# Optimization experiments

Measured on AMD Instinct MI355X. Metric: run time of the kernel, lower is better.

Reference implementation:

```python
import jax, jax.numpy as jnp
import numpy as np

G = 32          # grid size passed to FlashKAN
K_DEG = 3       # cubic B-splines
LO, HI = -3.0, 3.0

def make_knots():
    h = (HI - LO) / G
    # extended uniform knot vector: G + 2k + 1 knots -> G + k = 35 cubic basis fns
    return jnp.asarray(np.linspace(LO - K_DEG * h, HI + K_DEG * h, G + 2 * K_DEG + 1), jnp.float32)

def bspline_basis(x, knots):
    # Cox-de Boor, vectorized over all leading dims; loop only over degree (3 iters)
    xe = jnp.clip(x, LO, HI - 1e-4)[..., None]
    b = ((xe >= knots[:-1]) & (xe < knots[1:])).astype(x.dtype)  # degree-0 indicators
    for d in range(1, K_DEG + 1):
        left = (xe - knots[:-(d + 1)]) / (knots[d:-1] - knots[:-(d + 1)]) * b[..., :-1]
        right = (knots[d + 1:] - xe) / (knots[d + 1:] - knots[1:-d]) * b[..., 1:]
        b = left + right
    return b  # [..., E, G+K_DEG]

def kan(x, w_base, w_sp, knots):
    # FlashKAN layer: SiLU base branch + B-spline branch
    base = jax.nn.silu(x) @ w_base                          # [..., E] @ [E, O]
    spline = jnp.einsum('bleg,ego->blo', bspline_basis(x, knots), w_sp)
    return base + spline

def reference(query, key, value, wq_base, wq_sp, wk_base, wk_sp, wv_base, wv_sp):
    B, L, E = query.shape
    S = key.shape[-2]
    H = 8
    Dh = E // H
    knots = make_knots()
    Q = kan(query, wq_base, wq_sp, knots).reshape(B, L, H, Dh).transpose(0, 2, 1, 3)
    K = kan(key, wk_base, wk_sp, knots).reshape(B, S, H, Dh).transpose(0, 2, 1, 3)
    V = kan(value, wv_base, wv_sp, knots).reshape(B, S, H, Dh).transpose(0, 2, 1, 3)
    # no softmax, dropout p=0 -> (Q @ K^T) @ V == Q @ (K^T @ V), use O(L*d^2) form
    KtV = jnp.einsum('bhsd,bhse->bhde', K, V)               # [B,H,Dh,Dh]
    out = jnp.einsum('bhld,bhde->bhle', Q, KtV)             # [B,H,L,Dh]
    return out.transpose(0, 2, 1, 3).reshape(B, L, E)

def setup_inputs():
    key = jax.random.key(0)
    ks = jax.random.split(key, 9)
    B, L, E, NB = 2, 1024, 512, G + K_DEG
    sp_scale = 0.1 / np.sqrt(E)
    base_scale = 1.0 / np.sqrt(E)
    return {
        'query': jax.random.normal(ks[0], (B, L, E), jnp.float32),
        'key': jax.random.normal(ks[1], (B, L, E), jnp.float32),
        'value': jax.random.normal(ks[2], (B, L, E), jnp.float32),
        'wq_base': jax.random.normal(ks[3], (E, E), jnp.float32) * base_scale,
        'wq_sp': jax.random.normal(ks[4], (E, NB, E), jnp.float32) * sp_scale,
        'wk_base': jax.random.normal(ks[5], (E, E), jnp.float32) * base_scale,
        'wk_sp': jax.random.normal(ks[6], (E, NB, E), jnp.float32) * sp_scale,
        'wv_base': jax.random.normal(ks[7], (E, E), jnp.float32) * base_scale,
        'wv_sp': jax.random.normal(ks[8], (E, NB, E), jnp.float32) * sp_scale,
    }
```

## Files before the change

### kernel.cpp

```cpp
#include <hip/hip_runtime.h>
#include <hip/hip_bf16.h>
#include <stdint.h>

#define E_DIM 512
#define GNB   35
#define KSP   17920
#define KAUG  18432
#define MTOK  2048
#define BKW   128
#define NWIN  144
#define WINB  140
#define BM    128
#define BN    128
#define RB    256

typedef __attribute__((ext_vector_type(8))) short  short8;
typedef __attribute__((ext_vector_type(4))) short  short4v;
typedef __attribute__((ext_vector_type(4))) float  floatx4;

__device__ __forceinline__ short f2bf(float f) {
  __hip_bfloat16 h = __float2bfloat16(f);
  return *reinterpret_cast<short*>(&h);
}
__device__ __forceinline__ float silu_f(float x) { return x / (1.0f + __expf(-x)); }

__device__ __forceinline__ void gload_lds16(const void* g, void* l) {
  typedef const __attribute__((address_space(1))) void* gp_t;
  typedef __attribute__((address_space(3))) void* lp_t;
  __builtin_amdgcn_global_load_lds((gp_t)g, (lp_t)l, 16, 0, 0);
}

__device__ __forceinline__ int swz(int row, int byte_off) {
  return row * RB + (byte_off ^ ((row & 7) << 4));
}

__global__ __launch_bounds__(256) void wconv_kernel(
    const float* __restrict__ wq_sp, const float* __restrict__ wq_base,
    const float* __restrict__ wk_sp, const float* __restrict__ wk_base,
    const float* __restrict__ wv_sp, const float* __restrict__ wv_base,
    __hip_bfloat16* __restrict__ waugT)
{
  __shared__ float tile[64][65];
  const int tz = blockIdx.z;
  const float* wsp = tz == 0 ? wq_sp : (tz == 1 ? wk_sp : wv_sp);
  const float* wb  = tz == 0 ? wq_base : (tz == 1 ? wk_base : wv_base);
  const int k0 = blockIdx.x * 64;
  const int o0 = blockIdx.y * 64;
  const int t  = threadIdx.x;
#pragma unroll
  for (int it = 0; it < 16; ++it) {
    int idx = it * 256 + t;
    int r = idx >> 6, c = idx & 63;
    int k = k0 + r;
    float val = (k < KSP) ? wsp[(size_t)k * E_DIM + (o0 + c)]
                          : wb[(size_t)(k - KSP) * E_DIM + (o0 + c)];
    tile[r][c] = val;
  }
  __syncthreads();
  __hip_bfloat16* dst = waugT + (size_t)tz * E_DIM * KAUG;
#pragma unroll
  for (int it = 0; it < 16; ++it) {
    int idx = it * 256 + t;
    int r = idx >> 6, c = idx & 63;
    dst[(size_t)(o0 + r) * KAUG + (k0 + c)] = __float2bfloat16(tile[c][r]);
  }
}

template<int MODE>
__global__ __launch_bounds__(256) void kan_gemm(
    const float* __restrict__ q, const float* __restrict__ k_in,
    const float* __restrict__ v, const __hip_bfloat16* __restrict__ waugT,
    const float* __restrict__ wq_sp, const float* __restrict__ wq_base,
    const float* __restrict__ wk_sp, const float* __restrict__ wk_base,
    const float* __restrict__ wv_sp, const float* __restrict__ wv_base,
    float* __restrict__ C)
{
  __shared__ int4 sAq[BM * 16];
  __shared__ int4 sBq[BN * 16];
  char* pA = (char*)sAq;
  char* pB = (char*)sBq;

  const int z  = blockIdx.z;
  const int tz = z >> 2;
  const int ks = z & 3;
  const float* X = tz == 0 ? q : (tz == 1 ? k_in : v);
  const float* Wsp = tz == 0 ? wq_sp : (tz == 1 ? wk_sp : wv_sp);
  const float* Wb  = tz == 0 ? wq_base : (tz == 1 ? wk_base : wv_base);
  const char* WTb = (const char*)(waugT + (size_t)tz * E_DIM * KAUG);
  float* Cout = C + (size_t)tz * MTOK * E_DIM;

  const int m0 = blockIdx.x * BM;
  const int n0 = blockIdx.y * BN;
  const int t = threadIdx.x;
  const int lane = t & 63, wid = t >> 6;
  const int wm = wid >> 1, wn = wid & 1;
  const int fr = lane & 15, kg = lane >> 4;

  floatx4 acc[4][4];
  const floatx4 zf = {0.f, 0.f, 0.f, 0.f};
#pragma unroll
  for (int i = 0; i < 4; ++i)
#pragma unroll
    for (int j = 0; j < 4; ++j) acc[i][j] = zf;

  const int w_lo = ks * (NWIN / 4), w_hi = w_lo + (NWIN / 4);
  for (int win = w_lo; win < w_hi; ++win) {
    const int k0 = win * BKW;
    const bool spline = (win < WINB);
    __syncthreads();

    if (MODE == 0) {
      const int rB = t >> 4;
      const int cb = (t & 15) * 16;
#pragma unroll
      for (int p = 0; p < 8; ++p) {
        int row = p * 16 + rB;
        size_t goff = ((size_t)(n0 + row) * KAUG + k0) * 2
                    + (size_t)(cb ^ ((row & 7) << 4));
        gload_lds16(WTb + goff, pB + row * RB + cb);
      }
    } else {
      const float* Wrow = spline ? Wsp : Wb;
      const int koff0 = spline ? k0 : k0 - KSP;
      const int g  = t & 31;
      const int rg = t >> 5;
#pragma unroll
      for (int p = 0; p < 4; ++p) {
        const int r0 = (p * 8 + rg) * 4;
        float rv[4][4];
#pragma unroll
        for (int j = 0; j < 4; ++j) {
          const float* src = &Wrow[(size_t)(koff0 + r0 + j) * E_DIM + n0 + g];
#pragma unroll
          for (int j2 = 0; j2 < 4; ++j2) rv[j][j2] = src[32 * j2];
        }
#pragma unroll
        for (int j2 = 0; j2 < 4; ++j2) {
          const int nloc = g + 32 * j2;
          short4v sv;
          sv.x = f2bf(rv[0][j2]); sv.y = f2bf(rv[1][j2]);
          sv.z = f2bf(rv[2][j2]); sv.w = f2bf(rv[3][j2]);
          *(short4v*)&pB[swz(nloc, 2 * r0)] = sv;
        }
      }
    }

    if (spline) {
      const int4 z4 = make_int4(0, 0, 0, 0);
#pragma unroll
      for (int p = 0; p < 8; ++p) sAq[p * 256 + t] = z4;
      __syncthreads();
      const int elo = k0 / GNB;
      int ehi = (k0 + BKW - 1) / GNB; if (ehi > 511) ehi = 511;
      const int ne = ehi - elo + 1;
      const int npairs = BM * ne;
      for (int p = t; p < npairs; p += 256) {
        int m, ei;
        if (ne == 4) { m = p >> 2; ei = p & 3; }
        else         { m = (p * 52429) >> 18; ei = p - m * 5; }
        const int e = elo + ei;
        float x = X[(size_t)(m0 + m) * E_DIM + e];
        x = fminf(fmaxf(x, -3.0f), 3.0f - 1e-4f);
        float u = (x + 3.0f) * (16.0f / 3.0f);
        int ii = (int)u; ii = ii > 31 ? 31 : ii;
        float tt = u - (float)ii;
        float omt = 1.0f - tt;
        float t2 = tt * tt, t3 = t2 * tt;
        float b0 = omt * omt * omt * (1.0f / 6.0f);
        float b1 = (3.0f * t3 - 6.0f * t2 + 4.0f) * (1.0f / 6.0f);
        float b2 = (-3.0f * t3 + 3.0f * t2 + 3.0f * tt + 1.0f) * (1.0f / 6.0f);
        float b3 = t3 * (1.0f / 6.0f);
        const int c = e * GNB + ii - k0;
        if (c >= 0     && c < BKW)     *(short*)&pA[swz(m, 2 * c)]       = f2bf(b0);
        if (c + 1 >= 0 && c + 1 < BKW) *(short*)&pA[swz(m, 2 * (c + 1))] = f2bf(b1);
        if (c + 2 >= 0 && c + 2 < BKW) *(short*)&pA[swz(m, 2 * (c + 2))] = f2bf(b2);
        if (c + 3 >= 0 && c + 3 < BKW) *(short*)&pA[swz(m, 2 * (c + 3))] = f2bf(b3);
      }
    } else {
      const int e0 = k0 - KSP;
#pragma unroll
      for (int p = 0; p < 16; ++p) {
        int idx = p * 256 + t;
        int m = idx >> 5, c4 = idx & 31;
        floatx4 xv = *(const floatx4*)&X[(size_t)(m0 + m) * E_DIM + e0 + c4 * 4];
        short4v pk;
        pk.x = f2bf(silu_f(xv.x)); pk.y = f2bf(silu_f(xv.y));
        pk.z = f2bf(silu_f(xv.z)); pk.w = f2bf(silu_f(xv.w));
        *(short4v*)&pA[swz(m, 8 * c4)] = pk;
      }
    }
    __syncthreads();

#pragma unroll
    for (int kc = 0; kc < 4; ++kc) {
      const int kb = kc * 64 + kg * 16;
      short8 af[4], bfv[4];
#pragma unroll
      for (int fm = 0; fm < 4; ++fm) {
        const int row = wm * 64 + fm * 16 + fr;
        af[fm] = *(const short8*)&pA[swz(row, kb)];
      }
#pragma unroll
      for (int fn = 0; fn < 4; ++fn) {
        const int col = wn * 64 + fn * 16 + fr;
        bfv[fn] = *(const short8*)&pB[swz(col, kb)];
      }
#pragma unroll
      for (int fm = 0; fm < 4; ++fm)
#pragma unroll
        for (int fn = 0; fn < 4; ++fn)
          acc[fm][fn] = __builtin_amdgcn_mfma_f32_16x16x32_bf16(
              af[fm], bfv[fn], acc[fm][fn], 0, 0, 0);
    }
  }

  const int rowb = kg * 4;
#pragma unroll
  for (int fm = 0; fm < 4; ++fm)
#pragma unroll
    for (int fn = 0; fn < 4; ++fn)
#pragma unroll
      for (int r = 0; r < 4; ++r)
        atomicAdd(&Cout[(size_t)(m0 + wm * 64 + fm * 16 + rowb + r) * E_DIM
                        + (n0 + wn * 64 + fn * 16 + fr)],
                  acc[fm][fn][r]);
}

__global__ __launch_bounds__(256) void ktv_kernel(const float* __restrict__ C,
                                                  float* __restrict__ KtV)
{
  __shared__ float Ks[64][64];
  __shared__ float Vs[64][64];
  const int sc = blockIdx.x, bh = blockIdx.y;
  const int b = bh >> 3, h = bh & 7;
  const int t = threadIdx.x;
  const size_t base = ((size_t)(b * 1024 + sc * 64)) * E_DIM + h * 64;
  const float* Kp = C + (size_t)MTOK * E_DIM + base;
  const float* Vp = C + (size_t)2 * MTOK * E_DIM + base;
#pragma unroll
  for (int p = 0; p < 16; ++p) {
    int idx = p * 256 + t;
    int r = idx >> 6, c = idx & 63;
    Ks[r][c] = Kp[(size_t)r * E_DIM + c];
    Vs[r][c] = Vp[(size_t)r * E_DIM + c];
  }
  __syncthreads();
  const int d0 = (t & 15) * 4, e0 = (t >> 4) * 4;
  float acc[4][4] = {};
  for (int s = 0; s < 64; ++s) {
    float4 kv = *(const float4*)&Ks[s][d0];
    float4 vv = *(const float4*)&Vs[s][e0];
    float ka[4] = {kv.x, kv.y, kv.z, kv.w};
    float va[4] = {vv.x, vv.y, vv.z, vv.w};
#pragma unroll
    for (int i = 0; i < 4; ++i)
#pragma unroll
      for (int j = 0; j < 4; ++j) acc[i][j] = __fmaf_rn(ka[i], va[j], acc[i][j]);
  }
  float* dst = KtV + (size_t)bh * 4096;
#pragma unroll
  for (int i = 0; i < 4; ++i)
#pragma unroll
    for (int j = 0; j < 4; ++j)
      atomicAdd(&dst[(d0 + i) * 64 + (e0 + j)], acc[i][j]);
}

__global__ __launch_bounds__(256) void qktv_kernel(const float* __restrict__ C,
                                                   const float* __restrict__ KtV,
                                                   float* __restrict__ out)
{
  __shared__ float Qs[128][64];
  __shared__ float Ms[64][64];
  const int lt = blockIdx.x, bh = blockIdx.y;
  const int b = bh >> 3, h = bh & 7;
  const int t = threadIdx.x;
  const float* Qp = C + ((size_t)(b * 1024 + lt * 128)) * E_DIM + h * 64;
#pragma unroll
  for (int p = 0; p < 32; ++p) {
    int idx = p * 256 + t;
    Qs[idx >> 6][idx & 63] = Qp[(size_t)(idx >> 6) * E_DIM + (idx & 63)];
  }
#pragma unroll
  for (int p = 0; p < 16; ++p) {
    int idx = p * 256 + t;
    Ms[idx >> 6][idx & 63] = KtV[(size_t)bh * 4096 + idx];
  }
  __syncthreads();
  const int e0 = (t & 15) * 4;
  const int l0 = (t >> 4) * 8;
  float acc[8][4] = {};
  for (int d = 0; d < 64; ++d) {
    float4 mv = *(const float4*)&Ms[d][e0];
    float ma[4] = {mv.x, mv.y, mv.z, mv.w};
#pragma unroll
    for (int i = 0; i < 8; ++i) {
      float qv = Qs[l0 + i][d];
#pragma unroll
      for (int j = 0; j < 4; ++j) acc[i][j] = __fmaf_rn(qv, ma[j], acc[i][j]);
    }
  }
  float* op = out + ((size_t)(b * 1024 + lt * 128)) * E_DIM + h * 64;
#pragma unroll
  for (int i = 0; i < 8; ++i)
#pragma unroll
    for (int j = 0; j < 4; ++j)
      op[(size_t)(l0 + i) * E_DIM + (e0 + j)] = acc[i][j];
}

extern "C" void kernel_launch(void* const* d_in, const int* in_sizes, int n_in,
                              void* d_out, int out_size, void* d_ws, size_t ws_size,
                              hipStream_t stream) {
  const float* q   = (const float*)d_in[0];
  const float* k   = (const float*)d_in[1];
  const float* v   = (const float*)d_in[2];
  const float* wqb = (const float*)d_in[3];
  const float* wqs = (const float*)d_in[4];
  const float* wkb = (const float*)d_in[5];
  const float* wks = (const float*)d_in[6];
  const float* wvb = (const float*)d_in[7];
  const float* wvs = (const float*)d_in[8];

  char* ws = (char*)d_ws;
  const size_t WAUG_BYTES = (size_t)3 * E_DIM * KAUG * sizeof(__hip_bfloat16);
  const size_t C_BYTES    = (size_t)3 * MTOK * E_DIM * sizeof(float);
  const size_t KTV_BYTES  = (size_t)16 * 64 * 64 * sizeof(float);
  const bool full = ws_size >= WAUG_BYTES + C_BYTES + KTV_BYTES;
  float* C;
  float* KtV;
  __hip_bfloat16* waugT = (__hip_bfloat16*)ws;
  if (full) { C = (float*)(ws + WAUG_BYTES); KtV = (float*)(ws + WAUG_BYTES + C_BYTES); }
  else      { C = (float*)ws;                KtV = (float*)(ws + C_BYTES); }

  hipMemsetAsync(C, 0, C_BYTES, stream);
  hipMemsetAsync(KtV, 0, KTV_BYTES, stream);

  if (full) {
    wconv_kernel<<<dim3(KAUG / 64, E_DIM / 64, 3), 256, 0, stream>>>(
        wqs, wqb, wks, wkb, wvs, wvb, waugT);
    kan_gemm<0><<<dim3(MTOK / BM, E_DIM / BN, 12), 256, 0, stream>>>(
        q, k, v, waugT, wqs, wqb, wks, wkb, wvs, wvb, C);
  } else {
    kan_gemm<1><<<dim3(MTOK / BM, E_DIM / BN, 12), 256, 0, stream>>>(
        q, k, v, waugT, wqs, wqb, wks, wkb, wvs, wvb, C);
  }
  ktv_kernel<<<dim3(16, 16), 256, 0, stream>>>(C, KtV);
  qktv_kernel<<<dim3(8, 16), 256, 0, stream>>>(C, KtV, (float*)d_out);
}
```

Before: 431.7 us.

## Use k-slice LDS layout, XCD-aware block remap, vectorized weight conversion

Replaces the XOR-swizzled row-major LDS tiles with a k-slice-major layout, where each 8-element k chunk of all 128 rows is contiguous, so global_load_lds writes are linear per thread and MFMA fragment reads need no swizzle arithmetic. Flattens the GEMM grid to 1D and remaps block ids so consecutive blocks on the same XCD share weight and activation tiles for better L2 reuse. Vectorizes the weight conversion kernel with float4 loads and short4 bf16 stores. Replaces __syncthreads with explicit waitcnt plus s_barrier. The new layout may bring back LDS bank conflicts that the swizzle used to avoid.

```diff
diff --git a/kernel.cpp b/kernel.cpp
--- a/kernel.cpp
+++ b/kernel.cpp
@@ -12,7 +12,6 @@
 #define WINB  140
 #define BM    128
 #define BN    128
-#define RB    256
 
 typedef __attribute__((ext_vector_type(8))) short  short8;
 typedef __attribute__((ext_vector_type(4))) short  short4v;
@@ -30,9 +29,7 @@
   __builtin_amdgcn_global_load_lds((gp_t)g, (lp_t)l, 16, 0, 0);
 }
 
-__device__ __forceinline__ int swz(int row, int byte_off) {
-  return row * RB + (byte_off ^ ((row & 7) << 4));
-}
+__device__ __forceinline__ int kofs(int sl) { return ((sl >> 2) << 5) + ((sl & 3) << 3); }
 
 __global__ __launch_bounds__(256) void wconv_kernel(
     const float* __restrict__ wq_sp, const float* __restrict__ wq_base,
@@ -47,22 +44,26 @@
   const int k0 = blockIdx.x * 64;
   const int o0 = blockIdx.y * 64;
   const int t  = threadIdx.x;
-#pragma unroll
-  for (int it = 0; it < 16; ++it) {
+  const float* srcb = (k0 < KSP) ? wsp + (size_t)k0 * E_DIM
+                                 : wb + (size_t)(k0 - KSP) * E_DIM;
+#pragma unroll
+  for (int it = 0; it < 4; ++it) {
     int idx = it * 256 + t;
-    int r = idx >> 6, c = idx & 63;
-    int k = k0 + r;
-    float val = (k < KSP) ? wsp[(size_t)k * E_DIM + (o0 + c)]
-                          : wb[(size_t)(k - KSP) * E_DIM + (o0 + c)];
-    tile[r][c] = val;
+    int r = idx >> 4, c4 = (idx & 15) * 4;
+    floatx4 v = *(const floatx4*)&srcb[(size_t)r * E_DIM + o0 + c4];
+    tile[r][c4] = v.x; tile[r][c4 + 1] = v.y;
+    tile[r][c4 + 2] = v.z; tile[r][c4 + 3] = v.w;
   }
   __syncthreads();
   __hip_bfloat16* dst = waugT + (size_t)tz * E_DIM * KAUG;
 #pragma unroll
-  for (int it = 0; it < 16; ++it) {
+  for (int it = 0; it < 4; ++it) {
     int idx = it * 256 + t;
-    int r = idx >> 6, c = idx & 63;
-    dst[(size_t)(o0 + r) * KAUG + (k0 + c)] = __float2bfloat16(tile[c][r]);
+    int ro = idx >> 4, kc = (idx & 15) * 4;
+    short4v s;
+    s.x = f2bf(tile[kc][ro]);     s.y = f2bf(tile[kc + 1][ro]);
+    s.z = f2bf(tile[kc + 2][ro]); s.w = f2bf(tile[kc + 3][ro]);
+    *(short4v*)&dst[(size_t)(o0 + ro) * KAUG + k0 + kc] = s;
   }
 }
 
@@ -75,22 +76,25 @@
     const float* __restrict__ wv_sp, const float* __restrict__ wv_base,
     float* __restrict__ C)
 {
-  __shared__ int4 sAq[BM * 16];
-  __shared__ int4 sBq[BN * 16];
-  char* pA = (char*)sAq;
-  char* pB = (char*)sBq;
-
-  const int z  = blockIdx.z;
+  __shared__ char pA[32768];
+  __shared__ char pB[32768];
+
+  const int bid = blockIdx.x;
+  const int lid = (bid & 7) * 96 + (bid >> 3);
+  const int mx = lid & 15;
+  const int ny = (lid >> 4) & 3;
+  const int z  = lid >> 6;
   const int tz = z >> 2;
   const int ks = z & 3;
+
   const float* X = tz == 0 ? q : (tz == 1 ? k_in : v);
   const float* Wsp = tz == 0 ? wq_sp : (tz == 1 ? wk_sp : wv_sp);
   const float* Wb  = tz == 0 ? wq_base : (tz == 1 ? wk_base : wv_base);
   const char* WTb = (const char*)(waugT + (size_t)tz * E_DIM * KAUG);
   float* Cout = C + (size_t)tz * MTOK * E_DIM;
 
-  const int m0 = blockIdx.x * BM;
-  const int n0 = blockIdx.y * BN;
+  const int m0 = mx * BM;
+  const int n0 = ny * BN;
   const int t = threadIdx.x;
   const int lane = t & 63, wid = t >> 6;
   const int wm = wid >> 1, wn = wid & 1;
@@ -102,6 +106,9 @@
   for (int i = 0; i < 4; ++i)
 #pragma unroll
     for (int j = 0; j < 4; ++j) acc[i][j] = zf;
+
+  const int colt = t & 127;
+  const int slhi = t >> 7;
 
   const int w_lo = ks * (NWIN / 4), w_hi = w_lo + (NWIN / 4);
   for (int win = w_lo; win < w_hi; ++win) {
@@ -110,14 +117,11 @@
     __syncthreads();
 
     if (MODE == 0) {
-      const int rB = t >> 4;
-      const int cb = (t & 15) * 16;
 #pragma unroll
       for (int p = 0; p < 8; ++p) {
-        int row = p * 16 + rB;
-        size_t goff = ((size_t)(n0 + row) * KAUG + k0) * 2
-                    + (size_t)(cb ^ ((row & 7) << 4));
-        gload_lds16(WTb + goff, pB + row * RB + cb);
+        const int sl = 2 * p + slhi;
+        size_t goff = ((size_t)(n0 + colt) * KAUG + k0 + kofs(sl)) * 2;
+        gload_lds16(WTb + goff, pB + p * 4096 + t * 16);
       }
     } else {
       const float* Wrow = spline ? Wsp : Wb;
@@ -127,6 +131,7 @@
 #pragma unroll
       for (int p = 0; p < 4; ++p) {
         const int r0 = (p * 8 + rg) * 4;
+        const int sl = ((r0 >> 5) << 2) | ((r0 >> 3) & 3);
         float rv[4][4];
 #pragma unroll
         for (int j = 0; j < 4; ++j) {
@@ -140,7 +145,7 @@
           short4v sv;
           sv.x = f2bf(rv[0][j2]); sv.y = f2bf(rv[1][j2]);
           sv.z = f2bf(rv[2][j2]); sv.w = f2bf(rv[3][j2]);
-          *(short4v*)&pB[swz(nloc, 2 * r0)] = sv;
+          *(short4v*)&pB[sl * 2048 + nloc * 16 + (r0 & 7) * 2] = sv;
         }
       }
     }
@@ -148,8 +153,9 @@
     if (spline) {
       const int4 z4 = make_int4(0, 0, 0, 0);
 #pragma unroll
-      for (int p = 0; p < 8; ++p) sAq[p * 256 + t] = z4;
-      __syncthreads();
+      for (int p = 0; p < 8; ++p) ((int4*)pA)[p * 256 + t] = z4;
+      asm volatile("s_waitcnt lgkmcnt(0)" ::: "memory");
+      __builtin_amdgcn_s_barrier();
       const int elo = k0 / GNB;
       int ehi = (k0 + BKW - 1) / GNB; if (ehi > 511) ehi = 511;
       const int ne = ehi - elo + 1;
@@ -166,45 +172,54 @@
         float tt = u - (float)ii;
         float omt = 1.0f - tt;
         float t2 = tt * tt, t3 = t2 * tt;
-        float b0 = omt * omt * omt * (1.0f / 6.0f);
-        float b1 = (3.0f * t3 - 6.0f * t2 + 4.0f) * (1.0f / 6.0f);
-        float b2 = (-3.0f * t3 + 3.0f * t2 + 3.0f * tt + 1.0f) * (1.0f / 6.0f);
-        float b3 = t3 * (1.0f / 6.0f);
+        float w4[4];
+        w4[0] = omt * omt * omt * (1.0f / 6.0f);
+        w4[1] = (3.0f * t3 - 6.0f * t2 + 4.0f) * (1.0f / 6.0f);
+        w4[2] = (-3.0f * t3 + 3.0f * t2 + 3.0f * tt + 1.0f) * (1.0f / 6.0f);
+        w4[3] = t3 * (1.0f / 6.0f);
         const int c = e * GNB + ii - k0;
-        if (c >= 0     && c < BKW)     *(short*)&pA[swz(m, 2 * c)]       = f2bf(b0);
-        if (c + 1 >= 0 && c + 1 < BKW) *(short*)&pA[swz(m, 2 * (c + 1))] = f2bf(b1);
-        if (c + 2 >= 0 && c + 2 < BKW) *(short*)&pA[swz(m, 2 * (c + 2))] = f2bf(b2);
-        if (c + 3 >= 0 && c + 3 < BKW) *(short*)&pA[swz(m, 2 * (c + 3))] = f2bf(b3);
+#pragma unroll
+        for (int j = 0; j < 4; ++j) {
+          const int k = c + j;
+          if (k >= 0 && k < BKW) {
+            const int sl = ((k >> 5) << 2) | ((k >> 3) & 3);
+            *(short*)&pA[sl * 2048 + m * 16 + (k & 7) * 2] = f2bf(w4[j]);
+          }
+        }
       }
     } else {
       const int e0 = k0 - KSP;
 #pragma unroll
-      for (int p = 0; p < 16; ++p) {
-        int idx = p * 256 + t;
-        int m = idx >> 5, c4 = idx & 31;
-        floatx4 xv = *(const floatx4*)&X[(size_t)(m0 + m) * E_DIM + e0 + c4 * 4];
-        short4v pk;
-        pk.x = f2bf(silu_f(xv.x)); pk.y = f2bf(silu_f(xv.y));
-        pk.z = f2bf(silu_f(xv.z)); pk.w = f2bf(silu_f(xv.w));
-        *(short4v*)&pA[swz(m, 8 * c4)] = pk;
+      for (int p = 0; p < 8; ++p) {
+        const int id = p * 256 + t;
+        const int m = id & 127, sl = id >> 7;
+        const float* xs = &X[(size_t)(m0 + m) * E_DIM + e0 + kofs(sl)];
+        floatx4 a = *(const floatx4*)xs;
+        floatx4 b = *(const floatx4*)(xs + 4);
+        short8 pk;
+        pk[0] = f2bf(silu_f(a.x)); pk[1] = f2bf(silu_f(a.y));
+        pk[2] = f2bf(silu_f(a.z)); pk[3] = f2bf(silu_f(a.w));
+        pk[4] = f2bf(silu_f(b.x)); pk[5] = f2bf(silu_f(b.y));
+        pk[6] = f2bf(silu_f(b.z)); pk[7] = f2bf(silu_f(b.w));
+        *(short8*)&pA[sl * 2048 + m * 16] = pk;
       }
     }
-    __syncthreads();
-
+    asm volatile("s_waitcnt vmcnt(0) lgkmcnt(0)" ::: "memory");
+    __builtin_amdgcn_s_barrier();
+
+    const int arow = (wm * 64 + fr) * 16;
+    const int brow = (wn * 64 + fr) * 16;
+    const int sbase = kg * 2048;
 #pragma unroll
     for (int kc = 0; kc < 4; ++kc) {
-      const int kb = kc * 64 + kg * 16;
+      const int so = sbase + kc * 8192;
       short8 af[4], bfv[4];
 #pragma unroll
-      for (int fm = 0; fm < 4; ++fm) {
-        const int row = wm * 64 + fm * 16 + fr;
-        af[fm] = *(const short8*)&pA[swz(row, kb)];
-      }
-#pragma unroll
-      for (int fn = 0; fn < 4; ++fn) {
-        const int col = wn * 64 + fn * 16 + fr;
-        bfv[fn] = *(const short8*)&pB[swz(col, kb)];
-      }
+      for (int fm = 0; fm < 4; ++fm)
+        af[fm] = *(const short8*)&pA[so + arow + fm * 256];
+#pragma unroll
+      for (int fn = 0; fn < 4; ++fn)
+        bfv[fn] = *(const short8*)&pB[so + brow + fn * 256];
 #pragma unroll
       for (int fm = 0; fm < 4; ++fm)
 #pragma unroll
@@ -325,6 +340,7 @@
   const size_t C_BYTES    = (size_t)3 * MTOK * E_DIM * sizeof(float);
   const size_t KTV_BYTES  = (size_t)16 * 64 * 64 * sizeof(float);
   const bool full = ws_size >= WAUG_BYTES + C_BYTES + KTV_BYTES;
+
   float* C;
   float* KtV;
   __hip_bfloat16* waugT = (__hip_bfloat16*)ws;
@@ -337,10 +353,10 @@
   if (full) {
     wconv_kernel<<<dim3(KAUG / 64, E_DIM / 64, 3), 256, 0, stream>>>(
         wqs, wqb, wks, wkb, wvs, wvb, waugT);
-    kan_gemm<0><<<dim3(MTOK / BM, E_DIM / BN, 12), 256, 0, stream>>>(
+    kan_gemm<0><<<dim3(768), 256, 0, stream>>>(
         q, k, v, waugT, wqs, wqb, wks, wkb, wvs, wvb, C);
   } else {
-    kan_gemm<1><<<dim3(MTOK / BM, E_DIM / BN, 12), 256, 0, stream>>>(
+    kan_gemm<1><<<dim3(768), 256, 0, stream>>>(
         q, k, v, waugT, wqs, wqb, wks, wkb, wvs, wvb, C);
   }
   ktv_kernel<<<dim3(16, 16), 256, 0, stream>>>(C, KtV);
```

Result: slower. 440.8 us (+2.1%).
